# Optimization experiments

Hardware: AMD Instinct MI355X
Metric: run time of the kernel (lower is better)

## Reference

```python
import jax, jax.numpy as jnp
import numpy as np
import math

QB = 128.0  # 2**(8-1)
EPS = 1e-5

def _sign_ste(u):
    return u + jax.lax.stop_gradient(jnp.sign(u) - u)

def _clip_ste(u, lo, hi):
    return u + jax.lax.stop_gradient(jnp.clip(u, lo, hi) - u)

def bitlinear(x, w):
    # BitLinear with before_activation=False. w: [out, inp]
    alpha = w.mean()
    quant_w = _sign_ste(w - alpha)
    # F.layer_norm(x, x.size()[1:]): normalize over all dims except dim 0, eps=1e-5, no affine
    axes = tuple(range(1, x.ndim))
    mu = x.mean(axis=axes, keepdims=True)
    var = x.var(axis=axes, keepdims=True)
    x_norm = (x - mu) / jnp.sqrt(var + 1e-5)
    gamma = jnp.max(jnp.abs(x))
    beta = jnp.abs(w).sum() / (w.shape[0] * w.shape[1])
    scale = beta * gamma / QB
    quant_x = _clip_ste(x_norm * QB / gamma, -QB + EPS, QB - EPS)
    return jnp.einsum('...i,oi->...o', quant_x, quant_w) * scale

def setup_inputs() -> dict:
    key = jax.random.key(0)
    k1, k2, k3 = jax.random.split(key, 3)
    B, T, C = 4, 1024, 1024
    x = jax.random.normal(k1, (B, T, C), dtype=jnp.float32)
    # kaiming_uniform_(a=sqrt(5)) -> U(-b, b), b = sqrt(6/((1+5)*fan_in)) = 1/sqrt(fan_in)
    bnd = 1.0 / math.sqrt(C)
    w_in = jax.random.uniform(k2, (3 * C, C), dtype=jnp.float32, minval=-bnd, maxval=bnd)
    w_out = jax.random.uniform(k3, (C, C), dtype=jnp.float32, minval=-bnd, maxval=bnd)
    return {"x": x, "w_in": w_in, "w_out": w_out}

def reference(x, w_in, w_out):
    B, T, C = x.shape
    n_head = 16
    hd = C // n_head
    qkv = bitlinear(x, w_in)  # [B, T, 3C]
    q, k, v = jnp.split(qkv, 3, axis=2)
    q = q.reshape(B, T, n_head, hd).transpose(0, 2, 1, 3)  # [B,H,T,hd]
    k = k.reshape(B, T, n_head, hd).transpose(0, 2, 1, 3)
    v = v.reshape(B, T, n_head, hd).transpose(0, 2, 1, 3)
    att = jnp.einsum('bhqd,bhkd->bhqk', q, k) * (1.0 / math.sqrt(hd))
    causal = jnp.tril(jnp.ones((T, T), dtype=bool))
    att = jnp.where(causal[None, None], att, -jnp.inf)
    att = jax.nn.softmax(att, axis=-1)
    y = jnp.einsum('bhqk,bhkd->bhqd', att, v)
    y = y.transpose(0, 2, 1, 3).reshape(B, T, C)
    return bitlinear(y, w_out)
```

## Files before the change

### kernel.cpp

```cpp
#include <hip/hip_runtime.h>
#include <math.h>

#define B_   4
#define T_   1024
#define C_   1024
#define BT_  4096
#define NH_  16
#define HD_  64
#define QB_F 128.0f
#define EPS_F 1e-5f
#define KACT 1024

#define SLOT_SUMW_IN   0
#define SLOT_SUMW_OUT  2
#define SLOT_GAMMA_X   4
#define SLOT_GAMMA_Y   5
#define SLOT_SUMX      8
#define SLOT_SUMSQX    12
#define SLOT_SUMY      16
#define SLOT_SUMSQY    20

typedef __attribute__((ext_vector_type(8))) _Float16 half8;
typedef __attribute__((ext_vector_type(4))) _Float16 half4;
typedef __attribute__((ext_vector_type(4))) float    f32x4;

__device__ __forceinline__ unsigned short f2h(float f) {
    union { _Float16 h; unsigned short u; } cv; cv.h = (_Float16)f; return cv.u;
}


__global__ void reduce_w_kernel(const float* __restrict__ w, int n4,
                                float* __restrict__ sums)
{
    float s = 0.f, sa = 0.f;
    const int stride = gridDim.x * blockDim.x;
    for (int i = blockIdx.x * blockDim.x + threadIdx.x; i < n4; i += stride) {
        float4 v = ((const float4*)w)[i];
        s  += v.x + v.y + v.z + v.w;
        sa += fabsf(v.x) + fabsf(v.y) + fabsf(v.z) + fabsf(v.w);
    }
    #pragma unroll
    for (int o = 32; o > 0; o >>= 1) {
        s  += __shfl_down(s, o);
        sa += __shfl_down(sa, o);
    }
    __shared__ float sm[8];
    const int lane = threadIdx.x & 63, wid = threadIdx.x >> 6;
    if (lane == 0) { sm[wid] = s; sm[4 + wid] = sa; }
    __syncthreads();
    if (threadIdx.x == 0) {
        atomicAdd(&sums[0], sm[0] + sm[1] + sm[2] + sm[3]);
        atomicAdd(&sums[1], sm[4] + sm[5] + sm[6] + sm[7]);
    }
}

__global__ void reduce_x_kernel(const float* __restrict__ x, float* __restrict__ scal,
                                int sum_base, int sumsq_base, int gamma_slot)
{
    const int b = blockIdx.y;
    const float4* xb = (const float4*)(x + (size_t)b * T_ * C_);
    const int n4 = T_ * C_ / 4;
    float s = 0.f, ss = 0.f, am = 0.f;
    const int stride = gridDim.x * blockDim.x;
    for (int i = blockIdx.x * blockDim.x + threadIdx.x; i < n4; i += stride) {
        float4 v = xb[i];
        s  += v.x + v.y + v.z + v.w;
        ss += v.x*v.x + v.y*v.y + v.z*v.z + v.w*v.w;
        am = fmaxf(am, fmaxf(fmaxf(fabsf(v.x), fabsf(v.y)),
                             fmaxf(fabsf(v.z), fabsf(v.w))));
    }
    #pragma unroll
    for (int o = 32; o > 0; o >>= 1) {
        s  += __shfl_down(s, o);
        ss += __shfl_down(ss, o);
        am  = fmaxf(am, __shfl_down(am, o));
    }
    __shared__ float sm[12];
    const int lane = threadIdx.x & 63, wid = threadIdx.x >> 6;
    if (lane == 0) { sm[wid] = s; sm[4 + wid] = ss; sm[8 + wid] = am; }
    __syncthreads();
    if (threadIdx.x == 0) {
        atomicAdd(&scal[sum_base + b],   sm[0] + sm[1] + sm[2] + sm[3]);
        atomicAdd(&scal[sumsq_base + b], sm[4] + sm[5] + sm[6] + sm[7]);
        float m = fmaxf(fmaxf(sm[8], sm[9]), fmaxf(sm[10], sm[11]));
        atomicMax((unsigned int*)&scal[gamma_slot], __float_as_uint(m));
    }
}

__global__ void quant_act_kernel(const float* __restrict__ src, unsigned short* __restrict__ dst,
                                 const float* __restrict__ scal,
                                 int sum_base, int sumsq_base, int gamma_slot)
{
    const int n4 = BT_ * C_ / 4;
    const int stride = gridDim.x * blockDim.x;
    const float gamma = scal[gamma_slot];
    const float invTC = 1.0f / (float)(T_ * C_);
    const float qlo = -QB_F + EPS_F, qhi = QB_F - EPS_F;
    for (int i = blockIdx.x * blockDim.x + threadIdx.x; i < n4; i += stride) {
        const int row = i >> 8;
        const int k   = (i & 255) * 4;
        const int b   = row >> 10;
        const float mu  = scal[sum_base + b] * invTC;
        const float var = scal[sumsq_base + b] * invTC - mu * mu;
        const float am  = (QB_F / gamma) / sqrtf(var + EPS_F);
        float4 v = ((const float4*)src)[i];
        half4 hi;
        hi[0] = (_Float16)fminf(fmaxf((v.x - mu) * am, qlo), qhi);
        hi[1] = (_Float16)fminf(fmaxf((v.y - mu) * am, qlo), qhi);
        hi[2] = (_Float16)fminf(fmaxf((v.z - mu) * am, qlo), qhi);
        hi[3] = (_Float16)fminf(fmaxf((v.w - mu) * am, qlo), qhi);
        *(half4*)&dst[(size_t)row * KACT + k] = hi;
    }
}

__global__ void quant_w_kernel(const float* __restrict__ w, unsigned short* __restrict__ dst,
                               const float* __restrict__ scal, int sumw_slot, float inv_nw,
                               int n4)
{
    const float alpha = scal[sumw_slot] * inv_nw;
    const int stride = gridDim.x * blockDim.x;
    for (int i = blockIdx.x * blockDim.x + threadIdx.x; i < n4; i += stride) {
        const int row = i >> 8;
        const int k   = (i & 255) * 4;
        float4 v = ((const float4*)w)[i];
        half4 s;
        s[0] = (v.x > alpha) ? (_Float16)1.0f : ((v.x < alpha) ? (_Float16)-1.0f : (_Float16)0.0f);
        s[1] = (v.y > alpha) ? (_Float16)1.0f : ((v.y < alpha) ? (_Float16)-1.0f : (_Float16)0.0f);
        s[2] = (v.z > alpha) ? (_Float16)1.0f : ((v.z < alpha) ? (_Float16)-1.0f : (_Float16)0.0f);
        s[3] = (v.w > alpha) ? (_Float16)1.0f : ((v.w < alpha) ? (_Float16)-1.0f : (_Float16)0.0f);
        *(half4*)&dst[(size_t)row * KACT + k] = s;
    }
}


__device__ __forceinline__ void gload_lds16(const void* g, void* l)
{
    __builtin_amdgcn_global_load_lds(
        (const __attribute__((address_space(1))) unsigned int*)g,
        (__attribute__((address_space(3))) unsigned int*)l, 16, 0, 0);
}

__global__ __launch_bounds__(256) void mfma_gemm_kernel(
    const unsigned short* __restrict__ A,
    const unsigned short* __restrict__ Bm,
    float* __restrict__ Out,
    unsigned short* __restrict__ OutH,
    unsigned short* __restrict__ VtG,
    const float* __restrict__ scal, int N,
    int sumw_slot, int gamma_slot, float inv_nw)
{
    __shared__ __attribute__((aligned(16))) unsigned short As[128 * 32];
    __shared__ __attribute__((aligned(16))) unsigned short Bs[128 * 32];

    const int tid  = threadIdx.x;
    const int row0 = blockIdx.y * 128;
    const int col0 = blockIdx.x * 128;

    const float beta  = scal[sumw_slot + 1] * inv_nw;
    const float gamma = scal[gamma_slot];
    const float out_scale = beta * gamma / QB_F;

    const int wid = tid >> 6, lane = tid & 63;
    const int wr = (wid >> 1) * 64, wc = (wid & 1) * 64;
    const int lrow = lane & 15, lk = (lane >> 4) * 8;

    const int c0r = tid >> 2;
    const int c0k = (tid & 3) * 8;

    f32x4 acc[4][4];
    #pragma unroll
    for (int m = 0; m < 4; ++m)
        #pragma unroll
        for (int n = 0; n < 4; ++n)
            acc[m][n] = (f32x4){0.f, 0.f, 0.f, 0.f};

    for (int kt = 0; kt < KACT; kt += 32) {
        __syncthreads();
        gload_lds16(&A [(size_t)(row0 +      c0r) * KACT + kt + c0k], &As[c0r * 32 + c0k]);
        gload_lds16(&A [(size_t)(row0 + 64 + c0r) * KACT + kt + c0k], &As[(64 + c0r) * 32 + c0k]);
        gload_lds16(&Bm[(size_t)(col0 +      c0r) * KACT + kt + c0k], &Bs[c0r * 32 + c0k]);
        gload_lds16(&Bm[(size_t)(col0 + 64 + c0r) * KACT + kt + c0k], &Bs[(64 + c0r) * 32 + c0k]);
        __syncthreads();

        half8 a[4], b[4];
        #pragma unroll
        for (int m = 0; m < 4; ++m)
            a[m] = *(const half8*)&As[(wr + m * 16 + lrow) * 32 + lk];
        #pragma unroll
        for (int n = 0; n < 4; ++n)
            b[n] = *(const half8*)&Bs[(wc + n * 16 + lrow) * 32 + lk];
        #pragma unroll
        for (int m = 0; m < 4; ++m)
            #pragma unroll
            for (int n = 0; n < 4; ++n)
                acc[m][n] = __builtin_amdgcn_mfma_f32_16x16x32_f16(a[m], b[n], acc[m][n], 0, 0, 0);
    }

    const int orow = (lane >> 4) * 4;
    const int ocol = lane & 15;
    #pragma unroll
    for (int m = 0; m < 4; ++m) {
        const int gr0 = row0 + wr + m * 16 + orow;
        #pragma unroll
        for (int n = 0; n < 4; ++n) {
            const int c = col0 + wc + n * 16 + ocol;
            if (OutH) {
                if (c < 2 * C_) {
                    #pragma unroll
                    for (int q = 0; q < 4; ++q)
                        OutH[(size_t)(gr0 + q) * N + c] = f2h(acc[m][n][q] * out_scale);
                } else {
                    const int hh = (c - 2 * C_) >> 6, dd = (c - 2 * C_) & 63;
                    const int bb = gr0 >> 10,         tt = gr0 & 1023;
                    half4 hv;
                    hv[0] = (_Float16)(acc[m][n][0] * out_scale);
                    hv[1] = (_Float16)(acc[m][n][1] * out_scale);
                    hv[2] = (_Float16)(acc[m][n][2] * out_scale);
                    hv[3] = (_Float16)(acc[m][n][3] * out_scale);
                    *(half4*)&VtG[(((size_t)bb * NH_ + hh) * HD_ + dd) * T_ + tt] = hv;
                }
            } else {
                #pragma unroll
                for (int q = 0; q < 4; ++q)
                    Out[(size_t)(gr0 + q) * N + c] = acc[m][n][q] * out_scale;
            }
        }
    }
}

__global__ __launch_bounds__(512) void attn_mfma_kernel(
    const unsigned short* __restrict__ qkvH,
    const unsigned short* __restrict__ vtG,
    float* __restrict__ y, float* __restrict__ scal)
{
    __shared__ __attribute__((aligned(16))) unsigned short Kl[64 * 64];
    __shared__ __attribute__((aligned(16))) unsigned short Vl[64 * 64];
    __shared__ __attribute__((aligned(16))) unsigned short Pl[8][16 * 64];

    const int tid = threadIdx.x;
    const int qt = gridDim.x - 1 - blockIdx.x;
    const int h = blockIdx.y, b = blockIdx.z;
    const int q0 = qt * 128;
    const int wid = tid >> 6, lane = tid & 63;
    const int lq = lane & 15, lt = lane >> 4;
    const size_t rsH = 3 * C_;
    const unsigned short* qkvB = qkvH + (size_t)b * T_ * rsH + h * HD_;
    const unsigned short* vtB  = vtG + ((size_t)b * NH_ + h) * HD_ * T_;

    const int qrow = q0 + wid * 16 + lq;
    half8 qf[2];
    qf[0] = *(const half8*)&qkvB[(size_t)qrow * rsH + lt * 8];
    qf[1] = *(const half8*)&qkvB[(size_t)qrow * rsH + lt * 8 + 32];

    f32x4 accO[4];
    #pragma unroll
    for (int n = 0; n < 4; ++n) accO[n] = (f32x4){0.f, 0.f, 0.f, 0.f};
    float m_run = -1e30f, l_run = 0.f;

    unsigned short* Pw = &Pl[wid][0];

    const int strow = tid >> 3;
    const int sgr   = (((tid & 7) ^ (strow & 7)) << 3);

    const int nkt = 2 * qt + 2;
    for (int kt = 0; kt < nkt; ++kt) {
        const int k0 = kt * 64;
        __syncthreads();
        gload_lds16(&qkvB[(size_t)(k0 + strow) * rsH + C_ + sgr], &Kl[tid * 8]);
        gload_lds16(&vtB [(size_t)strow * T_ + k0 + sgr],         &Vl[tid * 8]);
        __syncthreads();

        f32x4 accS[4];
        #pragma unroll
        for (int m = 0; m < 4; ++m) accS[m] = (f32x4){0.f, 0.f, 0.f, 0.f};
        #pragma unroll
        for (int m = 0; m < 4; ++m) {
            const int rr = m * 16 + lq;
            const int rswz = (rr & 7) << 4;
            #pragma unroll
            for (int c = 0; c < 2; ++c) {
                half8 kf = *(const half8*)((const char*)Kl + ((rr * 128 + 64 * c + 16 * lt) ^ rswz));
                accS[m] = __builtin_amdgcn_mfma_f32_16x16x32_f16(kf, qf[c], accS[m], 0, 0, 0);
            }
        }

        float p[4][4];
        float mt = -1e30f;
        #pragma unroll
        for (int m = 0; m < 4; ++m)
            #pragma unroll
            for (int qq = 0; qq < 4; ++qq) {
                float s = accS[m][qq] * 0.125f;
                int kg = k0 + 16 * m + 4 * lt + qq;
                if (kg > qrow) s = -1e30f;
                p[m][qq] = s;
                mt = fmaxf(mt, s);
            }
        mt = fmaxf(mt, __shfl_xor(mt, 16));
        mt = fmaxf(mt, __shfl_xor(mt, 32));
        float mnew = fmaxf(m_run, mt);
        float sc = __expf(m_run - mnew);
        float ps = 0.f;
        #pragma unroll
        for (int m = 0; m < 4; ++m)
            #pragma unroll
            for (int qq = 0; qq < 4; ++qq) {
                float e = __expf(p[m][qq] - mnew);
                p[m][qq] = e;
                ps += e;
            }
        ps += __shfl_xor(ps, 16);
        ps += __shfl_xor(ps, 32);
        l_run = l_run * sc + ps;
        m_run = mnew;

        float srw[4];
        #pragma unroll
        for (int qq = 0; qq < 4; ++qq) srw[qq] = __shfl(sc, lt * 4 + qq);
        #pragma unroll
        for (int n = 0; n < 4; ++n) {
            accO[n][0] *= srw[0]; accO[n][1] *= srw[1];
            accO[n][2] *= srw[2]; accO[n][3] *= srw[3];
        }

        #pragma unroll
        for (int m = 0; m < 4; ++m) {
            half4 ph;
            ph[0] = (_Float16)p[m][0]; ph[1] = (_Float16)p[m][1];
            ph[2] = (_Float16)p[m][2]; ph[3] = (_Float16)p[m][3];
            *(half4*)((char*)Pw + ((lq * 128 + 32 * m + 8 * lt) ^ ((lq & 7) << 4))) = ph;
        }
        asm volatile("s_waitcnt lgkmcnt(0)" ::: "memory");
        __builtin_amdgcn_sched_barrier(0);

        #pragma unroll
        for (int c = 0; c < 2; ++c) {
            half8 pf = *(const half8*)((const char*)Pw + ((lq * 128 + 64 * c + 16 * lt) ^ ((lq & 7) << 4)));
            #pragma unroll
            for (int n = 0; n < 4; ++n) {
                const int dr = 16 * n + lq;
                half8 vf = *(const half8*)((const char*)Vl + ((dr * 128 + 64 * c + 16 * lt) ^ ((dr & 7) << 4)));
                accO[n] = __builtin_amdgcn_mfma_f32_16x16x32_f16(pf, vf, accO[n], 0, 0, 0);
            }
        }
    }

    float linv[4];
    #pragma unroll
    for (int qq = 0; qq < 4; ++qq) linv[qq] = 1.0f / __shfl(l_run, lt * 4 + qq);
    float s_loc = 0.f, ss_loc = 0.f, am_loc = 0.f;
    #pragma unroll
    for (int qq = 0; qq < 4; ++qq) {
        const size_t yrow = (size_t)(b * T_ + q0 + wid * 16 + lt * 4 + qq) * C_ + h * HD_;
        #pragma unroll
        for (int n = 0; n < 4; ++n) {
            float v = accO[n][qq] * linv[qq];
            y[yrow + 16 * n + lq] = v;
            s_loc += v; ss_loc += v * v; am_loc = fmaxf(am_loc, fabsf(v));
        }
    }
    #pragma unroll
    for (int o = 32; o > 0; o >>= 1) {
        s_loc  += __shfl_down(s_loc, o);
        ss_loc += __shfl_down(ss_loc, o);
        am_loc  = fmaxf(am_loc, __shfl_down(am_loc, o));
    }
    __syncthreads();
    float* red = (float*)&Pl[0][0];
    if (lane == 0) { red[wid] = s_loc; red[8 + wid] = ss_loc; red[16 + wid] = am_loc; }
    __syncthreads();
    if (tid == 0) {
        float s = 0.f, ss = 0.f, am = 0.f;
        #pragma unroll
        for (int i = 0; i < 8; ++i) {
            s += red[i]; ss += red[8 + i]; am = fmaxf(am, red[16 + i]);
        }
        atomicAdd(&scal[SLOT_SUMY + b], s);
        atomicAdd(&scal[SLOT_SUMSQY + b], ss);
        atomicMax((unsigned int*)&scal[SLOT_GAMMA_Y], __float_as_uint(am));
    }
}


extern "C" void kernel_launch(void* const* d_in, const int* in_sizes, int n_in,
                              void* d_out, int out_size, void* d_ws, size_t ws_size,
                              hipStream_t stream)
{
    (void)in_sizes; (void)n_in; (void)out_size; (void)ws_size;
    const float* x     = (const float*)d_in[0];
    const float* w_in  = (const float*)d_in[1];
    const float* w_out = (const float*)d_in[2];
    float* out  = (float*)d_out;

    float* scal = (float*)d_ws;
    unsigned short* qkvH = (unsigned short*)(scal + 64);
    unsigned short* vtG  = qkvH + (size_t)BT_ * 3 * C_;
    float* y = (float*)(vtG + (size_t)B_ * NH_ * HD_ * T_);
    unsigned short* Aq = (unsigned short*)(y + (size_t)BT_ * C_);
    unsigned short* Wq = Aq + (size_t)BT_ * KACT;

    hipMemsetAsync(d_ws, 0, 256, stream);

    reduce_w_kernel<<<dim3(256), 256, 0, stream>>>(w_in,  3 * C_ * C_ / 4, &scal[SLOT_SUMW_IN]);
    reduce_w_kernel<<<dim3(128), 256, 0, stream>>>(w_out, C_ * C_ / 4,     &scal[SLOT_SUMW_OUT]);
    reduce_x_kernel<<<dim3(128, B_), 256, 0, stream>>>(x, scal, SLOT_SUMX, SLOT_SUMSQX, SLOT_GAMMA_X);

    quant_act_kernel<<<dim3(1024), 256, 0, stream>>>(x, Aq, scal, SLOT_SUMX, SLOT_SUMSQX, SLOT_GAMMA_X);
    quant_w_kernel<<<dim3(1024), 256, 0, stream>>>(w_in, Wq, scal, SLOT_SUMW_IN,
                                                   1.0f / (float)(3 * C_ * C_), 3 * C_ * C_ / 4);

    mfma_gemm_kernel<<<dim3(3 * C_ / 128, BT_ / 128), 256, 0, stream>>>(
        Aq, Wq, nullptr, qkvH, vtG, scal, 3 * C_, SLOT_SUMW_IN, SLOT_GAMMA_X,
        1.0f / (float)(3 * C_ * C_));

    attn_mfma_kernel<<<dim3(T_ / 128, NH_, B_), 512, 0, stream>>>(qkvH, vtG, y, scal);

    quant_act_kernel<<<dim3(1024), 256, 0, stream>>>(y, Aq, scal, SLOT_SUMY, SLOT_SUMSQY, SLOT_GAMMA_Y);
    quant_w_kernel<<<dim3(512), 256, 0, stream>>>(w_out, Wq, scal, SLOT_SUMW_OUT,
                                                  1.0f / (float)(C_ * C_), C_ * C_ / 4);

    mfma_gemm_kernel<<<dim3(C_ / 128, BT_ / 128), 256, 0, stream>>>(
        Aq, Wq, out, nullptr, nullptr, scal, C_, SLOT_SUMW_OUT, SLOT_GAMMA_Y,
        1.0f / (float)(C_ * C_));
}
```

Baseline: 233.0 us.

## Fuse prologue reductions/quantization into two kernels and double-buffer attention K/V tiles

Merges the three reduction kernels into one stats kernel and the activation/weight quantization kernels (including w_out quantization) into one prep kernel, cutting launch count and letting independent work share the GPU. In the attention kernel, K/V tiles are now double-buffered in LDS so the next tile's global-to-LDS load is issued before computing on the current one, replacing two barriers per iteration with one. This costs extra LDS and workspace for a separate w_out quantized buffer.

```diff
diff --git a/kernel.cpp b/kernel.cpp
--- a/kernel.cpp
+++ b/kernel.cpp
@@ -28,62 +28,122 @@
     union { _Float16 h; unsigned short u; } cv; cv.h = (_Float16)f; return cv.u;
 }
 
-
-__global__ void reduce_w_kernel(const float* __restrict__ w, int n4,
-                                float* __restrict__ sums)
-{
-    float s = 0.f, sa = 0.f;
-    const int stride = gridDim.x * blockDim.x;
-    for (int i = blockIdx.x * blockDim.x + threadIdx.x; i < n4; i += stride) {
-        float4 v = ((const float4*)w)[i];
-        s  += v.x + v.y + v.z + v.w;
-        sa += fabsf(v.x) + fabsf(v.y) + fabsf(v.z) + fabsf(v.w);
-    }
-    #pragma unroll
-    for (int o = 32; o > 0; o >>= 1) {
-        s  += __shfl_down(s, o);
-        sa += __shfl_down(sa, o);
-    }
-    __shared__ float sm[8];
-    const int lane = threadIdx.x & 63, wid = threadIdx.x >> 6;
-    if (lane == 0) { sm[wid] = s; sm[4 + wid] = sa; }
-    __syncthreads();
-    if (threadIdx.x == 0) {
-        atomicAdd(&sums[0], sm[0] + sm[1] + sm[2] + sm[3]);
-        atomicAdd(&sums[1], sm[4] + sm[5] + sm[6] + sm[7]);
-    }
-}
-
-__global__ void reduce_x_kernel(const float* __restrict__ x, float* __restrict__ scal,
-                                int sum_base, int sumsq_base, int gamma_slot)
-{
-    const int b = blockIdx.y;
-    const float4* xb = (const float4*)(x + (size_t)b * T_ * C_);
-    const int n4 = T_ * C_ / 4;
-    float s = 0.f, ss = 0.f, am = 0.f;
-    const int stride = gridDim.x * blockDim.x;
-    for (int i = blockIdx.x * blockDim.x + threadIdx.x; i < n4; i += stride) {
-        float4 v = xb[i];
-        s  += v.x + v.y + v.z + v.w;
-        ss += v.x*v.x + v.y*v.y + v.z*v.z + v.w*v.w;
-        am = fmaxf(am, fmaxf(fmaxf(fabsf(v.x), fabsf(v.y)),
-                             fmaxf(fabsf(v.z), fabsf(v.w))));
-    }
-    #pragma unroll
-    for (int o = 32; o > 0; o >>= 1) {
-        s  += __shfl_down(s, o);
-        ss += __shfl_down(ss, o);
-        am  = fmaxf(am, __shfl_down(am, o));
-    }
+__global__ void stats_kernel(const float* __restrict__ x,
+                             const float* __restrict__ w_in,
+                             const float* __restrict__ w_out,
+                             float* __restrict__ scal)
+{
     __shared__ float sm[12];
-    const int lane = threadIdx.x & 63, wid = threadIdx.x >> 6;
-    if (lane == 0) { sm[wid] = s; sm[4 + wid] = ss; sm[8 + wid] = am; }
-    __syncthreads();
-    if (threadIdx.x == 0) {
-        atomicAdd(&scal[sum_base + b],   sm[0] + sm[1] + sm[2] + sm[3]);
-        atomicAdd(&scal[sumsq_base + b], sm[4] + sm[5] + sm[6] + sm[7]);
-        float m = fmaxf(fmaxf(sm[8], sm[9]), fmaxf(sm[10], sm[11]));
-        atomicMax((unsigned int*)&scal[gamma_slot], __float_as_uint(m));
+    const int tid = threadIdx.x;
+    const int lane = tid & 63, wid = tid >> 6;
+    const int gb = blockIdx.x;
+
+    if (gb < 384) {
+        const float* w; int n4, bi, nb; float* sums;
+        if (gb < 256) { w = w_in;  n4 = 3 * C_ * C_ / 4; bi = gb;      nb = 256; sums = &scal[SLOT_SUMW_IN]; }
+        else          { w = w_out; n4 = C_ * C_ / 4;     bi = gb - 256; nb = 128; sums = &scal[SLOT_SUMW_OUT]; }
+        float s = 0.f, sa = 0.f;
+        const int stride = nb * 256;
+        for (int i = bi * 256 + tid; i < n4; i += stride) {
+            float4 v = ((const float4*)w)[i];
+            s  += v.x + v.y + v.z + v.w;
+            sa += fabsf(v.x) + fabsf(v.y) + fabsf(v.z) + fabsf(v.w);
+        }
+        #pragma unroll
+        for (int o = 32; o > 0; o >>= 1) {
+            s  += __shfl_down(s, o);
+            sa += __shfl_down(sa, o);
+        }
+        if (lane == 0) { sm[wid] = s; sm[4 + wid] = sa; }
+        __syncthreads();
+        if (tid == 0) {
+            atomicAdd(&sums[0], sm[0] + sm[1] + sm[2] + sm[3]);
+            atomicAdd(&sums[1], sm[4] + sm[5] + sm[6] + sm[7]);
+        }
+    } else {
+        const int i0 = gb - 384;
+        const int b = i0 >> 7, bi = i0 & 127;
+        const float4* xb = (const float4*)(x + (size_t)b * T_ * C_);
+        const int n4 = T_ * C_ / 4;
+        float s = 0.f, ss = 0.f, am = 0.f;
+        const int stride = 128 * 256;
+        for (int i = bi * 256 + tid; i < n4; i += stride) {
+            float4 v = xb[i];
+            s  += v.x + v.y + v.z + v.w;
+            ss += v.x*v.x + v.y*v.y + v.z*v.z + v.w*v.w;
+            am = fmaxf(am, fmaxf(fmaxf(fabsf(v.x), fabsf(v.y)),
+                                 fmaxf(fabsf(v.z), fabsf(v.w))));
+        }
+        #pragma unroll
+        for (int o = 32; o > 0; o >>= 1) {
+            s  += __shfl_down(s, o);
+            ss += __shfl_down(ss, o);
+            am  = fmaxf(am, __shfl_down(am, o));
+        }
+        if (lane == 0) { sm[wid] = s; sm[4 + wid] = ss; sm[8 + wid] = am; }
+        __syncthreads();
+        if (tid == 0) {
+            atomicAdd(&scal[SLOT_SUMX + b],   sm[0] + sm[1] + sm[2] + sm[3]);
+            atomicAdd(&scal[SLOT_SUMSQX + b], sm[4] + sm[5] + sm[6] + sm[7]);
+            float m = fmaxf(fmaxf(sm[8], sm[9]), fmaxf(sm[10], sm[11]));
+            atomicMax((unsigned int*)&scal[SLOT_GAMMA_X], __float_as_uint(m));
+        }
+    }
+}
+
+__global__ void prep_kernel(const float* __restrict__ x,
+                            const float* __restrict__ w_in,
+                            const float* __restrict__ w_out,
+                            unsigned short* __restrict__ Aq,
+                            unsigned short* __restrict__ Wq,
+                            unsigned short* __restrict__ WqO,
+                            const float* __restrict__ scal)
+{
+    const int tid = threadIdx.x;
+    const int gb = blockIdx.x;
+
+    if (gb < 1024) {
+        const int n4 = BT_ * C_ / 4;
+        const int stride = 1024 * 256;
+        const float gamma = scal[SLOT_GAMMA_X];
+        const float invTC = 1.0f / (float)(T_ * C_);
+        const float qlo = -QB_F + EPS_F, qhi = QB_F - EPS_F;
+        for (int i = gb * 256 + tid; i < n4; i += stride) {
+            const int row = i >> 8;
+            const int k   = (i & 255) * 4;
+            const int b   = row >> 10;
+            const float mu  = scal[SLOT_SUMX + b] * invTC;
+            const float var = scal[SLOT_SUMSQX + b] * invTC - mu * mu;
+            const float am  = (QB_F / gamma) / sqrtf(var + EPS_F);
+            float4 v = ((const float4*)x)[i];
+            half4 hi;
+            hi[0] = (_Float16)fminf(fmaxf((v.x - mu) * am, qlo), qhi);
+            hi[1] = (_Float16)fminf(fmaxf((v.y - mu) * am, qlo), qhi);
+            hi[2] = (_Float16)fminf(fmaxf((v.z - mu) * am, qlo), qhi);
+            hi[3] = (_Float16)fminf(fmaxf((v.w - mu) * am, qlo), qhi);
+            *(half4*)&Aq[(size_t)row * KACT + k] = hi;
+        }
+    } else {
+        const float* w; unsigned short* dst; int n4, bi, nb; float alpha;
+        if (gb < 1792) {
+            w = w_in;  dst = Wq;  n4 = 3 * C_ * C_ / 4; bi = gb - 1024; nb = 768;
+            alpha = scal[SLOT_SUMW_IN] / (float)(3 * C_ * C_);
+        } else {
+            w = w_out; dst = WqO; n4 = C_ * C_ / 4;     bi = gb - 1792; nb = 256;
+            alpha = scal[SLOT_SUMW_OUT] / (float)(C_ * C_);
+        }
+        const int stride = nb * 256;
+        for (int i = bi * 256 + tid; i < n4; i += stride) {
+            const int row = i >> 8;
+            const int k   = (i & 255) * 4;
+            float4 v = ((const float4*)w)[i];
+            half4 s;
+            s[0] = (v.x > alpha) ? (_Float16)1.0f : ((v.x < alpha) ? (_Float16)-1.0f : (_Float16)0.0f);
+            s[1] = (v.y > alpha) ? (_Float16)1.0f : ((v.y < alpha) ? (_Float16)-1.0f : (_Float16)0.0f);
+            s[2] = (v.z > alpha) ? (_Float16)1.0f : ((v.z < alpha) ? (_Float16)-1.0f : (_Float16)0.0f);
+            s[3] = (v.w > alpha) ? (_Float16)1.0f : ((v.w < alpha) ? (_Float16)-1.0f : (_Float16)0.0f);
+            *(half4*)&dst[(size_t)row * KACT + k] = s;
+        }
     }
 }
 
@@ -110,25 +170,6 @@
         hi[2] = (_Float16)fminf(fmaxf((v.z - mu) * am, qlo), qhi);
         hi[3] = (_Float16)fminf(fmaxf((v.w - mu) * am, qlo), qhi);
         *(half4*)&dst[(size_t)row * KACT + k] = hi;
-    }
-}
-
-__global__ void quant_w_kernel(const float* __restrict__ w, unsigned short* __restrict__ dst,
-                               const float* __restrict__ scal, int sumw_slot, float inv_nw,
-                               int n4)
-{
-    const float alpha = scal[sumw_slot] * inv_nw;
-    const int stride = gridDim.x * blockDim.x;
-    for (int i = blockIdx.x * blockDim.x + threadIdx.x; i < n4; i += stride) {
-        const int row = i >> 8;
-        const int k   = (i & 255) * 4;
-        float4 v = ((const float4*)w)[i];
-        half4 s;
-        s[0] = (v.x > alpha) ? (_Float16)1.0f : ((v.x < alpha) ? (_Float16)-1.0f : (_Float16)0.0f);
-        s[1] = (v.y > alpha) ? (_Float16)1.0f : ((v.y < alpha) ? (_Float16)-1.0f : (_Float16)0.0f);
-        s[2] = (v.z > alpha) ? (_Float16)1.0f : ((v.z < alpha) ? (_Float16)-1.0f : (_Float16)0.0f);
-        s[3] = (v.w > alpha) ? (_Float16)1.0f : ((v.w < alpha) ? (_Float16)-1.0f : (_Float16)0.0f);
-        *(half4*)&dst[(size_t)row * KACT + k] = s;
     }
 }
 
@@ -233,8 +274,8 @@
     const unsigned short* __restrict__ vtG,
     float* __restrict__ y, float* __restrict__ scal)
 {
-    __shared__ __attribute__((aligned(16))) unsigned short Kl[64 * 64];
-    __shared__ __attribute__((aligned(16))) unsigned short Vl[64 * 64];
+    __shared__ __attribute__((aligned(16))) unsigned short Kl[2][64 * 64];
+    __shared__ __attribute__((aligned(16))) unsigned short Vl[2][64 * 64];
     __shared__ __attribute__((aligned(16))) unsigned short Pl[8][16 * 64];
 
     const int tid = threadIdx.x;
@@ -263,12 +304,18 @@
     const int sgr   = (((tid & 7) ^ (strow & 7)) << 3);
 
     const int nkt = 2 * qt + 2;
+    gload_lds16(&qkvB[(size_t)strow * rsH + C_ + sgr], &Kl[0][tid * 8]);
+    gload_lds16(&vtB [(size_t)strow * T_ + sgr],       &Vl[0][tid * 8]);
+    __syncthreads();
+
     for (int kt = 0; kt < nkt; ++kt) {
         const int k0 = kt * 64;
-        __syncthreads();
-        gload_lds16(&qkvB[(size_t)(k0 + strow) * rsH + C_ + sgr], &Kl[tid * 8]);
-        gload_lds16(&vtB [(size_t)strow * T_ + k0 + sgr],         &Vl[tid * 8]);
-        __syncthreads();
+        const int cur = kt & 1;
+        if (kt + 1 < nkt) {
+            const int kn = k0 + 64;
+            gload_lds16(&qkvB[(size_t)(kn + strow) * rsH + C_ + sgr], &Kl[cur ^ 1][tid * 8]);
+            gload_lds16(&vtB [(size_t)strow * T_ + kn + sgr],         &Vl[cur ^ 1][tid * 8]);
+        }
 
         f32x4 accS[4];
         #pragma unroll
@@ -279,7 +326,7 @@
             const int rswz = (rr & 7) << 4;
             #pragma unroll
             for (int c = 0; c < 2; ++c) {
-                half8 kf = *(const half8*)((const char*)Kl + ((rr * 128 + 64 * c + 16 * lt) ^ rswz));
+                half8 kf = *(const half8*)((const char*)&Kl[cur][0] + ((rr * 128 + 64 * c + 16 * lt) ^ rswz));
                 accS[m] = __builtin_amdgcn_mfma_f32_16x16x32_f16(kf, qf[c], accS[m], 0, 0, 0);
             }
         }
@@ -339,10 +386,11 @@
             #pragma unroll
             for (int n = 0; n < 4; ++n) {
                 const int dr = 16 * n + lq;
-                half8 vf = *(const half8*)((const char*)Vl + ((dr * 128 + 64 * c + 16 * lt) ^ ((dr & 7) << 4)));
+                half8 vf = *(const half8*)((const char*)&Vl[cur][0] + ((dr * 128 + 64 * c + 16 * lt) ^ ((dr & 7) << 4)));
                 accO[n] = __builtin_amdgcn_mfma_f32_16x16x32_f16(pf, vf, accO[n], 0, 0, 0);
             }
         }
+        __syncthreads();
     }
 
     float linv[4];
@@ -398,16 +446,12 @@
     float* y = (float*)(vtG + (size_t)B_ * NH_ * HD_ * T_);
     unsigned short* Aq = (unsigned short*)(y + (size_t)BT_ * C_);
     unsigned short* Wq = Aq + (size_t)BT_ * KACT;
+    unsigned short* WqO = Wq + (size_t)3 * C_ * KACT;
 
     hipMemsetAsync(d_ws, 0, 256, stream);
 
-    reduce_w_kernel<<<dim3(256), 256, 0, stream>>>(w_in,  3 * C_ * C_ / 4, &scal[SLOT_SUMW_IN]);
-    reduce_w_kernel<<<dim3(128), 256, 0, stream>>>(w_out, C_ * C_ / 4,     &scal[SLOT_SUMW_OUT]);
-    reduce_x_kernel<<<dim3(128, B_), 256, 0, stream>>>(x, scal, SLOT_SUMX, SLOT_SUMSQX, SLOT_GAMMA_X);
-
-    quant_act_kernel<<<dim3(1024), 256, 0, stream>>>(x, Aq, scal, SLOT_SUMX, SLOT_SUMSQX, SLOT_GAMMA_X);
-    quant_w_kernel<<<dim3(1024), 256, 0, stream>>>(w_in, Wq, scal, SLOT_SUMW_IN,
-                                                   1.0f / (float)(3 * C_ * C_), 3 * C_ * C_ / 4);
+    stats_kernel<<<dim3(896), 256, 0, stream>>>(x, w_in, w_out, scal);
+    prep_kernel<<<dim3(2048), 256, 0, stream>>>(x, w_in, w_out, Aq, Wq, WqO, scal);
 
     mfma_gemm_kernel<<<dim3(3 * C_ / 128, BT_ / 128), 256, 0, stream>>>(
         Aq, Wq, nullptr, qkvH, vtG, scal, 3 * C_, SLOT_SUMW_IN, SLOT_GAMMA_X,
@@ -416,10 +460,8 @@
     attn_mfma_kernel<<<dim3(T_ / 128, NH_, B_), 512, 0, stream>>>(qkvH, vtG, y, scal);
 
     quant_act_kernel<<<dim3(1024), 256, 0, stream>>>(y, Aq, scal, SLOT_SUMY, SLOT_SUMSQY, SLOT_GAMMA_Y);
-    quant_w_kernel<<<dim3(512), 256, 0, stream>>>(w_out, Wq, scal, SLOT_SUMW_OUT,
-                                                  1.0f / (float)(C_ * C_), C_ * C_ / 4);
 
     mfma_gemm_kernel<<<dim3(C_ / 128, BT_ / 128), 256, 0, stream>>>(
-        Aq, Wq, out, nullptr, nullptr, scal, C_, SLOT_SUMW_OUT, SLOT_GAMMA_Y,
+        Aq, WqO, out, nullptr, nullptr, scal, C_, SLOT_SUMW_OUT, SLOT_GAMMA_Y,
         1.0f / (float)(C_ * C_));
 }
```

After: 217.4 us. -6.7%, faster.
